# Performance work log

Measured on AMD Instinct MI355X. Metric: run time of the kernel, lower is better.

Reference implementation:

```python
import jax, jax.numpy as jnp
import numpy as np

NEAR, FAR, N_SAMPLES = 1.0, 6.0, 64
FAR_APPEND = 1000.0


def setup_inputs() -> dict:
    key = jax.random.key(0)
    ks = jax.random.split(key, 8)
    B, R = 2, 4096
    # pixel coords in a 128x128 image
    x_pix = jax.random.uniform(ks[0], (B, R, 2), dtype=jnp.float32) * 128.0
    # plausible pinhole intrinsics (fx=fy=128, cx=cy=64)
    K = jnp.array([[128.0, 0.0, 64.0], [0.0, 128.0, 64.0], [0.0, 0.0, 1.0]], dtype=jnp.float32)
    intrinsics = jnp.tile(K[None], (B, 1, 1))
    # identity rotation, small translation cam2world
    c2w = jnp.eye(4, dtype=jnp.float32).at[:3, 3].set(jnp.array([0.1, -0.2, 0.5]))
    cam2world = jnp.tile(c2w[None], (B, 1, 1))
    H = 256
    W1 = jax.random.normal(ks[1], (3, H), dtype=jnp.float32) / np.sqrt(3.0)
    b1 = jnp.zeros((H,), jnp.float32)
    W2 = jax.random.normal(ks[2], (H, H), dtype=jnp.float32) / np.sqrt(H)
    b2 = jnp.zeros((H,), jnp.float32)
    W3 = jax.random.normal(ks[3], (H, 4), dtype=jnp.float32) / np.sqrt(H)
    b3 = jnp.zeros((4,), jnp.float32)
    return {"x_pix": x_pix, "intrinsics": intrinsics, "cam2world": cam2world,
            "W1": W1, "b1": b1, "W2": W2, "b2": b2, "W3": W3, "b3": b3}


def _radiance_field(pts, W1, b1, W2, b2, W3, b3):
    # pts: (B, N, 3) -> sigma (B, N, 1), rad (B, N, 3)
    h = jax.nn.relu(pts @ W1 + b1)
    h = jax.nn.relu(h @ W2 + b2)
    o = h @ W3 + b3
    return jax.nn.relu(o[..., :1]), jax.nn.sigmoid(o[..., 1:])


def _get_world_rays(x_pix, intrinsics, cam2world):
    B, R, _ = x_pix.shape
    inv_K = jnp.linalg.inv(intrinsics)  # (B,3,3)
    xy_hom = jnp.concatenate([x_pix, jnp.ones((B, R, 1), x_pix.dtype)], axis=-1)  # (B,R,3)
    dirs_cam = jnp.einsum("bij,brj->bri", inv_K, xy_hom)  # unnormalized cam-frame dirs
    dirs_hom = jnp.concatenate([dirs_cam, jnp.zeros((B, R, 1), x_pix.dtype)], axis=-1)  # w=0 vector
    dirs_world = jnp.einsum("bij,brj->bri", cam2world, dirs_hom)[..., :3]
    origins = jnp.broadcast_to(cam2world[:, None, :3, 3], (B, R, 3))
    return origins, dirs_world


def _volume_integral(z_vals, sigmas, radiances):
    # z_vals: (S,); sigmas: (B,R,S,1); radiances: (B,R,S,3)
    dists = jnp.diff(z_vals, append=jnp.array([FAR_APPEND], z_vals.dtype))  # (S,)
    alpha = 1.0 - jnp.exp(-sigmas * dists[None, None, :, None])  # (B,R,S,1)
    Ts = jnp.cumprod(1.0 - alpha, axis=2)  # inclusive cumprod, matching torch
    weights = alpha * Ts  # (B,R,S,1)
    rgb = jnp.sum(weights * radiances, axis=2)  # (B,R,3)
    depth_map = jnp.einsum("brsv,s->brv", weights, z_vals)  # (B,R,1)
    return rgb, depth_map, weights


def reference(x_pix, intrinsics, cam2world, W1, b1, W2, b2, W3, b3):
    B, R = x_pix.shape[0], x_pix.shape[1]
    ros, rds = _get_world_rays(x_pix, intrinsics, cam2world)
    z_vals = jnp.linspace(NEAR, FAR, N_SAMPLES, dtype=x_pix.dtype)  # (S,)
    pts = ros[:, :, None, :] + rds[:, :, None, :] * z_vals[None, None, :, None]  # (B,R,S,3)
    pts = pts.reshape(B, -1, 3)
    sigma, rad = _radiance_field(pts, W1, b1, W2, b2, W3, b3)
    sigma = sigma.reshape(B, R, N_SAMPLES, 1)
    rad = rad.reshape(B, R, N_SAMPLES, 3)
    rgb, depth_map, weights = _volume_integral(z_vals, sigma, rad)
    accum = jnp.sum(weights, axis=-2)  # (B,R,1)
    rgb = rgb + (1.0 - accum)  # white background
    return rgb, depth_map
```

## Files before the change

kernel.cpp:

```cpp
#include <hip/hip_runtime.h>

typedef unsigned short u16;
typedef _Float16 f16x8 __attribute__((ext_vector_type(8)));
typedef float    f32x4  __attribute__((ext_vector_type(4)));
typedef float    f32x16 __attribute__((ext_vector_type(16)));

#define NRAYS 8192

#define WS_W2T  0
#define WS_B2   131072
#define WS_W3   132096
#define WS_B3   136192
#define WS_W1   136208
#define WS_B1   139280
#define WS_INTR 140304
#define WS_C2W  140384

__device__ __forceinline__ float bf2f(u16 u){
  union { unsigned int i; float f; } v; v.i = ((unsigned int)u) << 16; return v.f;
}
__device__ __forceinline__ u16 f2h(float f){
  union { _Float16 h; u16 u; } v; v.h = (_Float16)f;
  return v.u;
}
__device__ __forceinline__ int detect_bf16(const void* intr){
  return (((const u16*)intr)[0] == 0x4300u) ? 1 : 0;
}

__device__ __forceinline__ void conv_arr(const void* src, float* dst, int n, int bf, int tid){
  if (bf){
    const u16* s = (const u16*)src;
    for (int i = tid; i < n; i += 256) dst[i] = bf2f(s[i]);
  } else {
    const float* s = (const float*)src;
    for (int i = tid; i < n; i += 256) dst[i] = s[i];
  }
}

__global__ void prep(const void* __restrict__ W2, const void* __restrict__ W1,
                     const void* __restrict__ b1, const void* __restrict__ b2,
                     const void* __restrict__ W3, const void* __restrict__ b3,
                     const void* __restrict__ intr, const void* __restrict__ c2w,
                     char* __restrict__ ws)
{
  const int bf = detect_bf16(intr);
  const int t = threadIdx.x;
  if (blockIdx.x == 16){
    conv_arr(W1,  (float*)(ws + WS_W1),  768,  bf, t);
    conv_arr(b1,  (float*)(ws + WS_B1),  256,  bf, t);
    conv_arr(b2,  (float*)(ws + WS_B2),  256,  bf, t);
    conv_arr(W3,  (float*)(ws + WS_W3),  1024, bf, t);
    conv_arr(b3,  (float*)(ws + WS_B3),  4,    bf, t);
    conv_arr(intr,(float*)(ws + WS_INTR),18,   bf, t);
    conv_arr(c2w, (float*)(ws + WS_C2W), 32,   bf, t);
    return;
  }
  __shared__ u16 tile[64][72];
  const int bx = blockIdx.x & 3;
  const int by = blockIdx.x >> 2;
  const int c = t & 63, rb = t >> 6;
  u16* W2T = (u16*)(ws + WS_W2T);
  #pragma unroll
  for (int rr = 0; rr < 64; rr += 4){
    int k = bx*64 + rr + rb;
    int n = by*64 + c;
    float v = bf ? bf2f(((const u16*)W2)[k*256 + n]) : ((const float*)W2)[k*256 + n];
    tile[rr + rb][c] = f2h(v);
  }
  __syncthreads();
  #pragma unroll
  for (int rr = 0; rr < 64; rr += 4){
    int n = by*64 + rr + rb;
    int k = bx*64 + c;
    W2T[n*256 + k] = tile[c][rr + rb];
  }
}

__global__ __launch_bounds__(256, 2) void nerf_fused(
    const void* __restrict__ x_pix,
    const void* __restrict__ intr,
    const char* __restrict__ ws,
    float* __restrict__ out)
{
  __shared__ __align__(16) u16   h1s[128 * 256];
  __shared__ __align__(16) float obuf[4 * 128 * 4];

  const int tid = threadIdx.x;
  const int l   = tid & 63;
  const int w   = tid >> 6;
  const int ray = w >> 1;
  const int rayg = blockIdx.x * 2 + ray;
  const int bb   = rayg >> 12;
  const int bf   = detect_bf16(intr);

  const float* intrf = (const float*)(ws + WS_INTR);
  const float* c2wf  = (const float*)(ws + WS_C2W);
  const float* W1f   = (const float*)(ws + WS_W1);
  const float* b1f   = (const float*)(ws + WS_B1);
  const float* b2f   = (const float*)(ws + WS_B2);
  const float* W3f   = (const float*)(ws + WS_W3);
  const u16*   W2T   = (const u16*)(ws + WS_W2T);

  float px, py;
  if (bf){
    px = bf2f(((const u16*)x_pix)[rayg*2 + 0]);
    py = bf2f(((const u16*)x_pix)[rayg*2 + 1]);
  } else {
    px = ((const float*)x_pix)[rayg*2 + 0];
    py = ((const float*)x_pix)[rayg*2 + 1];
  }
  float Ka[9], Mm[16];
  #pragma unroll
  for (int i = 0; i < 9;  i++) Ka[i] = intrf[bb*9  + i];
  #pragma unroll
  for (int i = 0; i < 16; i++) Mm[i] = c2wf[bb*16 + i];
  float a = Ka[0], b_ = Ka[1], c = Ka[2];
  float d = Ka[3], e  = Ka[4], f = Ka[5];
  float g = Ka[6], h_ = Ka[7], i9 = Ka[8];
  float det = a*(e*i9 - f*h_) - b_*(d*i9 - f*g) + c*(d*h_ - e*g);
  float inv = 1.0f / det;
  float i00 = (e*i9 - f*h_)*inv, i01 = (c*h_ - b_*i9)*inv, i02 = (b_*f - c*e)*inv;
  float i10 = (f*g - d*i9)*inv, i11 = (a*i9 - c*g)*inv, i12 = (c*d - a*f)*inv;
  float i20 = (d*h_ - e*g)*inv, i21 = (b_*g - a*h_)*inv, i22 = (a*e - b_*d)*inv;
  float dcx = i00*px + i01*py + i02;
  float dcy = i10*px + i11*py + i12;
  float dcz = i20*px + i21*py + i22;
  float dx = Mm[0]*dcx + Mm[1]*dcy + Mm[2]*dcz;
  float dy = Mm[4]*dcx + Mm[5]*dcy + Mm[6]*dcz;
  float dz = Mm[8]*dcx + Mm[9]*dcy + Mm[10]*dcz;
  float ox = Mm[3], oy = Mm[7], oz = Mm[11];

  const int kbase = (w & 1)*128 + l*2;
  float aa0, aa1, gg0, gg1;
  {
    float2 r0 = *(const float2*)(W1f + kbase);
    float2 r1 = *(const float2*)(W1f + 256 + kbase);
    float2 r2 = *(const float2*)(W1f + 512 + kbase);
    float2 rb = *(const float2*)(b1f + kbase);
    aa0 = ox*r0.x + oy*r1.x + oz*r2.x + rb.x;
    aa1 = ox*r0.y + oy*r1.y + oz*r2.y + rb.y;
    gg0 = dx*r0.x + dy*r1.x + dz*r2.x;
    gg1 = dx*r0.y + dy*r1.y + dz*r2.y;
  }
  const float step = 5.0f / 63.0f;
  const int chunk_w = ((w & 1) << 4) + (l >> 2);
  const int sub_b   = (l & 3) << 2;
  {
    char* hb = (char*)h1s + (ray*64)*512;
    #pragma unroll 8
    for (int s = 0; s < 64; s++){
      float z = 1.0f + step * (float)s;
      u16 e0 = f2h(fmaxf(fmaf(gg0, z, aa0), 0.0f));
      u16 e1 = f2h(fmaxf(fmaf(gg1, z, aa1), 0.0f));
      unsigned pk = (unsigned)e0 | ((unsigned)e1 << 16);
      *(unsigned*)(hb + s*512 + ((chunk_w ^ (s & 7)) << 4) + sub_b) = pk;
    }
  }
  __syncthreads();

  const int l31 = l & 31;
  const int h   = l >> 5;
  const int m7  = l31 & 7;
  const int nbase = w * 64;

  f32x16 acc[2][4];
  #pragma unroll
  for (int nt = 0; nt < 2; nt++)
    #pragma unroll
    for (int mt = 0; mt < 4; mt++)
      acc[nt][mt] = (f32x16){0.f,0.f,0.f,0.f,0.f,0.f,0.f,0.f,
                             0.f,0.f,0.f,0.f,0.f,0.f,0.f,0.f};

  const u16* Arow = W2T + (nbase + l31)*256 + h*8;
  const char* hbase = (const char*)h1s;

  f16x8 a_cur[2];
  a_cur[0] = *(const f16x8*)(Arow);
  a_cur[1] = *(const f16x8*)(Arow + 32*256);

  #pragma unroll
  for (int t = 0; t < 16; t++){
    f16x8 a_nxt[2];
    if (t < 15){
      a_nxt[0] = *(const f16x8*)(Arow + (t+1)*16);
      a_nxt[1] = *(const f16x8*)(Arow + 32*256 + (t+1)*16);
    }
    const int swz = ((2*t + h) ^ m7) << 4;
    f16x8 bfr[4];
    #pragma unroll
    for (int mt = 0; mt < 4; mt++)
      bfr[mt] = *(const f16x8*)(hbase + (mt*32 + l31)*512 + swz);
    #pragma unroll
    for (int nt = 0; nt < 2; nt++)
      #pragma unroll
      for (int mt = 0; mt < 4; mt++)
        acc[nt][mt] = __builtin_amdgcn_mfma_f32_32x32x16_f16(
            a_cur[nt], bfr[mt], acc[nt][mt], 0, 0, 0);
    if (t < 15){ a_cur[0] = a_nxt[0]; a_cur[1] = a_nxt[1]; }
  }

  f32x4 o_m[4];
  #pragma unroll
  for (int mt = 0; mt < 4; mt++) o_m[mt] = (f32x4){0.f,0.f,0.f,0.f};

  #pragma unroll
  for (int nt = 0; nt < 2; nt++){
    #pragma unroll
    for (int gq = 0; gq < 4; gq++){
      const int n0 = nbase + nt*32 + gq*8 + h*4;
      f32x4 b2v = *(const f32x4*)(b2f + n0);
      f32x4 w30 = *(const f32x4*)(W3f + n0*4);
      f32x4 w31 = *(const f32x4*)(W3f + (n0+1)*4);
      f32x4 w32 = *(const f32x4*)(W3f + (n0+2)*4);
      f32x4 w33 = *(const f32x4*)(W3f + (n0+3)*4);
      #pragma unroll
      for (int mt = 0; mt < 4; mt++){
        float h0 = fmaxf(acc[nt][mt][gq*4+0] + b2v.x, 0.0f);
        float h1 = fmaxf(acc[nt][mt][gq*4+1] + b2v.y, 0.0f);
        float h2 = fmaxf(acc[nt][mt][gq*4+2] + b2v.z, 0.0f);
        float h3 = fmaxf(acc[nt][mt][gq*4+3] + b2v.w, 0.0f);
        o_m[mt] = o_m[mt] + h0*w30 + h1*w31 + h2*w32 + h3*w33;
      }
    }
  }

  #pragma unroll
  for (int mt = 0; mt < 4; mt++)
    #pragma unroll
    for (int j = 0; j < 4; j++){
      float v = o_m[mt][j];
      v += __shfl_xor(v, 32, 64);
      o_m[mt][j] = v;
    }

  if (h == 0){
    #pragma unroll
    for (int mt = 0; mt < 4; mt++)
      *(f32x4*)&obuf[(w*128 + mt*32 + l31)*4] = o_m[mt];
  }
  __syncthreads();

  if (w < 2){
    const int m = w*64 + l;
    const f32x4* ob4 = (const f32x4*)obuf;
    f32x4 oj  = ob4[m] + ob4[128 + m] + ob4[256 + m] + ob4[384 + m];
    f32x4 b3v = *(const f32x4*)(ws + WS_B3);
    float o_s0 = oj.x + b3v.x;
    float o_s1 = oj.y + b3v.y;
    float o_s2 = oj.z + b3v.z;
    float o_s3 = oj.w + b3v.w;

    const float zc    = 1.0f + step * (float)l;
    const float znext = (l == 63) ? 1000.0f : (1.0f + step * (float)(l + 1));
    const float dist  = znext - zc;
    float sigma = fmaxf(o_s0, 0.0f);
    float alpha = 1.0f - __expf(-sigma * dist);
    float t = 1.0f - alpha;
    #pragma unroll
    for (int sh = 1; sh < 64; sh <<= 1){
      float u = __shfl_up(t, sh, 64);
      if (l >= sh) t *= u;
    }
    float wgt = alpha * t;
    float r0 = 1.0f / (1.0f + __expf(-o_s1));
    float r1 = 1.0f / (1.0f + __expf(-o_s2));
    float r2 = 1.0f / (1.0f + __expf(-o_s3));
    float s0 = wgt*r0, s1 = wgt*r1, s2 = wgt*r2, sw = wgt, sz = wgt*zc;
    #pragma unroll
    for (int sh = 1; sh < 64; sh <<= 1){
      s0 += __shfl_xor(s0, sh, 64);
      s1 += __shfl_xor(s1, sh, 64);
      s2 += __shfl_xor(s2, sh, 64);
      sw += __shfl_xor(sw, sh, 64);
      sz += __shfl_xor(sz, sh, 64);
    }
    if (l == 0){
      const int rg = blockIdx.x*2 + w;
      float bg = 1.0f - sw;
      out[rg*3 + 0] = s0 + bg;
      out[rg*3 + 1] = s1 + bg;
      out[rg*3 + 2] = s2 + bg;
      out[3*NRAYS + rg] = sz;
    }
  }
}

extern "C" void kernel_launch(void* const* d_in, const int* in_sizes, int n_in,
                              void* d_out, int out_size, void* d_ws, size_t ws_size,
                              hipStream_t stream)
{
  const void* x_pix = d_in[0];
  const void* intr  = d_in[1];
  const void* c2w   = d_in[2];
  const void* W1    = d_in[3];
  const void* b1    = d_in[4];
  const void* W2    = d_in[5];
  const void* b2    = d_in[6];
  const void* W3    = d_in[7];
  const void* b3    = d_in[8];
  float* outp = (float*)d_out;
  char*  ws   = (char*)d_ws;

  hipLaunchKernelGGL(prep, dim3(17), dim3(256), 0, stream,
                     W2, W1, b1, b2, W3, b3, intr, c2w, ws);
  hipLaunchKernelGGL(nerf_fused, dim3(NRAYS/2), dim3(256), 0, stream,
                     x_pix, intr, ws, outp);
}
```

Before: 177.0 us.

## Make fused NeRF kernel persistent with W2 fragments held in registers

The launch shrinks from 4096 blocks to 512. Each block now loops over 8 ray pairs and loads its whole slice of the transposed W2 into registers once, instead of streaming it from global memory for every ray pair. The W1 and b1 slices are also hoisted out of the loop. The aim is to cut repeated weight traffic and per-block setup, at the cost of much higher register pressure (128 VGPRs of weights plus the accumulators) and less block-level parallelism to hide latency.

```diff
diff --git a/kernel.cpp b/kernel.cpp
--- a/kernel.cpp
+++ b/kernel.cpp
@@ -88,10 +88,7 @@
   const int tid = threadIdx.x;
   const int l   = tid & 63;
   const int w   = tid >> 6;
-  const int ray = w >> 1;
-  const int rayg = blockIdx.x * 2 + ray;
-  const int bb   = rayg >> 12;
-  const int bf   = detect_bf16(intr);
+  const int bf  = detect_bf16(intr);
 
   const float* intrf = (const float*)(ws + WS_INTR);
   const float* c2wf  = (const float*)(ws + WS_C2W);
@@ -101,186 +98,189 @@
   const float* W3f   = (const float*)(ws + WS_W3);
   const u16*   W2T   = (const u16*)(ws + WS_W2T);
 
-  float px, py;
-  if (bf){
-    px = bf2f(((const u16*)x_pix)[rayg*2 + 0]);
-    py = bf2f(((const u16*)x_pix)[rayg*2 + 1]);
-  } else {
-    px = ((const float*)x_pix)[rayg*2 + 0];
-    py = ((const float*)x_pix)[rayg*2 + 1];
-  }
-  float Ka[9], Mm[16];
-  #pragma unroll
-  for (int i = 0; i < 9;  i++) Ka[i] = intrf[bb*9  + i];
-  #pragma unroll
-  for (int i = 0; i < 16; i++) Mm[i] = c2wf[bb*16 + i];
-  float a = Ka[0], b_ = Ka[1], c = Ka[2];
-  float d = Ka[3], e  = Ka[4], f = Ka[5];
-  float g = Ka[6], h_ = Ka[7], i9 = Ka[8];
-  float det = a*(e*i9 - f*h_) - b_*(d*i9 - f*g) + c*(d*h_ - e*g);
-  float inv = 1.0f / det;
-  float i00 = (e*i9 - f*h_)*inv, i01 = (c*h_ - b_*i9)*inv, i02 = (b_*f - c*e)*inv;
-  float i10 = (f*g - d*i9)*inv, i11 = (a*i9 - c*g)*inv, i12 = (c*d - a*f)*inv;
-  float i20 = (d*h_ - e*g)*inv, i21 = (b_*g - a*h_)*inv, i22 = (a*e - b_*d)*inv;
-  float dcx = i00*px + i01*py + i02;
-  float dcy = i10*px + i11*py + i12;
-  float dcz = i20*px + i21*py + i22;
-  float dx = Mm[0]*dcx + Mm[1]*dcy + Mm[2]*dcz;
-  float dy = Mm[4]*dcx + Mm[5]*dcy + Mm[6]*dcz;
-  float dz = Mm[8]*dcx + Mm[9]*dcy + Mm[10]*dcz;
-  float ox = Mm[3], oy = Mm[7], oz = Mm[11];
-
-  const int kbase = (w & 1)*128 + l*2;
-  float aa0, aa1, gg0, gg1;
-  {
-    float2 r0 = *(const float2*)(W1f + kbase);
-    float2 r1 = *(const float2*)(W1f + 256 + kbase);
-    float2 r2 = *(const float2*)(W1f + 512 + kbase);
-    float2 rb = *(const float2*)(b1f + kbase);
-    aa0 = ox*r0.x + oy*r1.x + oz*r2.x + rb.x;
-    aa1 = ox*r0.y + oy*r1.y + oz*r2.y + rb.y;
-    gg0 = dx*r0.x + dy*r1.x + dz*r2.x;
-    gg1 = dx*r0.y + dy*r1.y + dz*r2.y;
-  }
-  const float step = 5.0f / 63.0f;
-  const int chunk_w = ((w & 1) << 4) + (l >> 2);
-  const int sub_b   = (l & 3) << 2;
-  {
-    char* hb = (char*)h1s + (ray*64)*512;
-    #pragma unroll 8
-    for (int s = 0; s < 64; s++){
-      float z = 1.0f + step * (float)s;
-      u16 e0 = f2h(fmaxf(fmaf(gg0, z, aa0), 0.0f));
-      u16 e1 = f2h(fmaxf(fmaf(gg1, z, aa1), 0.0f));
-      unsigned pk = (unsigned)e0 | ((unsigned)e1 << 16);
-      *(unsigned*)(hb + s*512 + ((chunk_w ^ (s & 7)) << 4) + sub_b) = pk;
-    }
-  }
-  __syncthreads();
-
   const int l31 = l & 31;
   const int h   = l >> 5;
   const int m7  = l31 & 7;
   const int nbase = w * 64;
 
-  f32x16 acc[2][4];
-  #pragma unroll
-  for (int nt = 0; nt < 2; nt++)
+  f16x8 aw[2][16];
+  {
+    const u16* Arow = W2T + (nbase + l31)*256 + h*8;
+    #pragma unroll
+    for (int nt = 0; nt < 2; nt++)
+      #pragma unroll
+      for (int kt = 0; kt < 16; kt++)
+        aw[nt][kt] = *(const f16x8*)(Arow + nt*32*256 + kt*16);
+  }
+
+  const int kbase = (w & 1)*128 + l*2;
+  const float2 r0 = *(const float2*)(W1f + kbase);
+  const float2 r1 = *(const float2*)(W1f + 256 + kbase);
+  const float2 r2 = *(const float2*)(W1f + 512 + kbase);
+  const float2 rbv = *(const float2*)(b1f + kbase);
+  const int chunk_w = ((w & 1) << 4) + (l >> 2);
+  const int sub_b   = (l & 3) << 2;
+  const float step = 5.0f / 63.0f;
+
+  #pragma unroll 1
+  for (int it = 0; it < 8; it++){
+    const int pr   = it*512 + blockIdx.x;
+    const int rayg = pr*2 + (w >> 1);
+    const int bb   = rayg >> 12;
+
+    float px, py;
+    if (bf){
+      px = bf2f(((const u16*)x_pix)[rayg*2 + 0]);
+      py = bf2f(((const u16*)x_pix)[rayg*2 + 1]);
+    } else {
+      px = ((const float*)x_pix)[rayg*2 + 0];
+      py = ((const float*)x_pix)[rayg*2 + 1];
+    }
+    float Ka[9], Mm[16];
+    #pragma unroll
+    for (int i = 0; i < 9;  i++) Ka[i] = intrf[bb*9  + i];
+    #pragma unroll
+    for (int i = 0; i < 16; i++) Mm[i] = c2wf[bb*16 + i];
+    float a = Ka[0], b_ = Ka[1], c = Ka[2];
+    float d = Ka[3], e  = Ka[4], f = Ka[5];
+    float g = Ka[6], h_ = Ka[7], i9 = Ka[8];
+    float det = a*(e*i9 - f*h_) - b_*(d*i9 - f*g) + c*(d*h_ - e*g);
+    float inv = 1.0f / det;
+    float i00 = (e*i9 - f*h_)*inv, i01 = (c*h_ - b_*i9)*inv, i02 = (b_*f - c*e)*inv;
+    float i10 = (f*g - d*i9)*inv, i11 = (a*i9 - c*g)*inv, i12 = (c*d - a*f)*inv;
+    float i20 = (d*h_ - e*g)*inv, i21 = (b_*g - a*h_)*inv, i22 = (a*e - b_*d)*inv;
+    float dcx = i00*px + i01*py + i02;
+    float dcy = i10*px + i11*py + i12;
+    float dcz = i20*px + i21*py + i22;
+    float dx = Mm[0]*dcx + Mm[1]*dcy + Mm[2]*dcz;
+    float dy = Mm[4]*dcx + Mm[5]*dcy + Mm[6]*dcz;
+    float dz = Mm[8]*dcx + Mm[9]*dcy + Mm[10]*dcz;
+    float ox = Mm[3], oy = Mm[7], oz = Mm[11];
+
+    float aa0 = ox*r0.x + oy*r1.x + oz*r2.x + rbv.x;
+    float aa1 = ox*r0.y + oy*r1.y + oz*r2.y + rbv.y;
+    float gg0 = dx*r0.x + dy*r1.x + dz*r2.x;
+    float gg1 = dx*r0.y + dy*r1.y + dz*r2.y;
+    {
+      char* hb = (char*)h1s + ((w >> 1)*64)*512;
+      #pragma unroll 8
+      for (int s = 0; s < 64; s++){
+        float z = 1.0f + step * (float)s;
+        u16 e0 = f2h(fmaxf(fmaf(gg0, z, aa0), 0.0f));
+        u16 e1 = f2h(fmaxf(fmaf(gg1, z, aa1), 0.0f));
+        unsigned pk = (unsigned)e0 | ((unsigned)e1 << 16);
+        *(unsigned*)(hb + s*512 + ((chunk_w ^ (s & 7)) << 4) + sub_b) = pk;
+      }
+    }
+    __syncthreads();
+
+    f32x16 acc[2][4];
+    #pragma unroll
+    for (int nt = 0; nt < 2; nt++)
+      #pragma unroll
+      for (int mt = 0; mt < 4; mt++)
+        acc[nt][mt] = (f32x16){0.f,0.f,0.f,0.f,0.f,0.f,0.f,0.f,
+                               0.f,0.f,0.f,0.f,0.f,0.f,0.f,0.f};
+
+    const char* hbase = (const char*)h1s;
+    #pragma unroll
+    for (int kt = 0; kt < 16; kt++){
+      const int swz = ((2*kt + h) ^ m7) << 4;
+      f16x8 bfr[4];
+      #pragma unroll
+      for (int mt = 0; mt < 4; mt++)
+        bfr[mt] = *(const f16x8*)(hbase + (mt*32 + l31)*512 + swz);
+      #pragma unroll
+      for (int nt = 0; nt < 2; nt++)
+        #pragma unroll
+        for (int mt = 0; mt < 4; mt++)
+          acc[nt][mt] = __builtin_amdgcn_mfma_f32_32x32x16_f16(
+              aw[nt][kt], bfr[mt], acc[nt][mt], 0, 0, 0);
+    }
+
+    f32x4 o_m[4];
+    #pragma unroll
+    for (int mt = 0; mt < 4; mt++) o_m[mt] = (f32x4){0.f,0.f,0.f,0.f};
+
+    #pragma unroll
+    for (int nt = 0; nt < 2; nt++){
+      #pragma unroll
+      for (int gq = 0; gq < 4; gq++){
+        const int n0 = nbase + nt*32 + gq*8 + h*4;
+        f32x4 b2v = *(const f32x4*)(b2f + n0);
+        f32x4 w30 = *(const f32x4*)(W3f + n0*4);
+        f32x4 w31 = *(const f32x4*)(W3f + (n0+1)*4);
+        f32x4 w32 = *(const f32x4*)(W3f + (n0+2)*4);
+        f32x4 w33 = *(const f32x4*)(W3f + (n0+3)*4);
+        #pragma unroll
+        for (int mt = 0; mt < 4; mt++){
+          float h0 = fmaxf(acc[nt][mt][gq*4+0] + b2v.x, 0.0f);
+          float h1 = fmaxf(acc[nt][mt][gq*4+1] + b2v.y, 0.0f);
+          float h2 = fmaxf(acc[nt][mt][gq*4+2] + b2v.z, 0.0f);
+          float h3 = fmaxf(acc[nt][mt][gq*4+3] + b2v.w, 0.0f);
+          o_m[mt] = o_m[mt] + h0*w30 + h1*w31 + h2*w32 + h3*w33;
+        }
+      }
+    }
+
     #pragma unroll
     for (int mt = 0; mt < 4; mt++)
-      acc[nt][mt] = (f32x16){0.f,0.f,0.f,0.f,0.f,0.f,0.f,0.f,
-                             0.f,0.f,0.f,0.f,0.f,0.f,0.f,0.f};
-
-  const u16* Arow = W2T + (nbase + l31)*256 + h*8;
-  const char* hbase = (const char*)h1s;
-
-  f16x8 a_cur[2];
-  a_cur[0] = *(const f16x8*)(Arow);
-  a_cur[1] = *(const f16x8*)(Arow + 32*256);
-
-  #pragma unroll
-  for (int t = 0; t < 16; t++){
-    f16x8 a_nxt[2];
-    if (t < 15){
-      a_nxt[0] = *(const f16x8*)(Arow + (t+1)*16);
-      a_nxt[1] = *(const f16x8*)(Arow + 32*256 + (t+1)*16);
-    }
-    const int swz = ((2*t + h) ^ m7) << 4;
-    f16x8 bfr[4];
-    #pragma unroll
-    for (int mt = 0; mt < 4; mt++)
-      bfr[mt] = *(const f16x8*)(hbase + (mt*32 + l31)*512 + swz);
-    #pragma unroll
-    for (int nt = 0; nt < 2; nt++)
+      #pragma unroll
+      for (int j = 0; j < 4; j++){
+        float v = o_m[mt][j];
+        v += __shfl_xor(v, 32, 64);
+        o_m[mt][j] = v;
+      }
+
+    if (h == 0){
       #pragma unroll
       for (int mt = 0; mt < 4; mt++)
-        acc[nt][mt] = __builtin_amdgcn_mfma_f32_32x32x16_f16(
-            a_cur[nt], bfr[mt], acc[nt][mt], 0, 0, 0);
-    if (t < 15){ a_cur[0] = a_nxt[0]; a_cur[1] = a_nxt[1]; }
-  }
-
-  f32x4 o_m[4];
-  #pragma unroll
-  for (int mt = 0; mt < 4; mt++) o_m[mt] = (f32x4){0.f,0.f,0.f,0.f};
-
-  #pragma unroll
-  for (int nt = 0; nt < 2; nt++){
-    #pragma unroll
-    for (int gq = 0; gq < 4; gq++){
-      const int n0 = nbase + nt*32 + gq*8 + h*4;
-      f32x4 b2v = *(const f32x4*)(b2f + n0);
-      f32x4 w30 = *(const f32x4*)(W3f + n0*4);
-      f32x4 w31 = *(const f32x4*)(W3f + (n0+1)*4);
-      f32x4 w32 = *(const f32x4*)(W3f + (n0+2)*4);
-      f32x4 w33 = *(const f32x4*)(W3f + (n0+3)*4);
-      #pragma unroll
-      for (int mt = 0; mt < 4; mt++){
-        float h0 = fmaxf(acc[nt][mt][gq*4+0] + b2v.x, 0.0f);
-        float h1 = fmaxf(acc[nt][mt][gq*4+1] + b2v.y, 0.0f);
-        float h2 = fmaxf(acc[nt][mt][gq*4+2] + b2v.z, 0.0f);
-        float h3 = fmaxf(acc[nt][mt][gq*4+3] + b2v.w, 0.0f);
-        o_m[mt] = o_m[mt] + h0*w30 + h1*w31 + h2*w32 + h3*w33;
-      }
-    }
-  }
-
-  #pragma unroll
-  for (int mt = 0; mt < 4; mt++)
-    #pragma unroll
-    for (int j = 0; j < 4; j++){
-      float v = o_m[mt][j];
-      v += __shfl_xor(v, 32, 64);
-      o_m[mt][j] = v;
-    }
-
-  if (h == 0){
-    #pragma unroll
-    for (int mt = 0; mt < 4; mt++)
-      *(f32x4*)&obuf[(w*128 + mt*32 + l31)*4] = o_m[mt];
-  }
-  __syncthreads();
-
-  if (w < 2){
-    const int m = w*64 + l;
-    const f32x4* ob4 = (const f32x4*)obuf;
-    f32x4 oj  = ob4[m] + ob4[128 + m] + ob4[256 + m] + ob4[384 + m];
-    f32x4 b3v = *(const f32x4*)(ws + WS_B3);
-    float o_s0 = oj.x + b3v.x;
-    float o_s1 = oj.y + b3v.y;
-    float o_s2 = oj.z + b3v.z;
-    float o_s3 = oj.w + b3v.w;
-
-    const float zc    = 1.0f + step * (float)l;
-    const float znext = (l == 63) ? 1000.0f : (1.0f + step * (float)(l + 1));
-    const float dist  = znext - zc;
-    float sigma = fmaxf(o_s0, 0.0f);
-    float alpha = 1.0f - __expf(-sigma * dist);
-    float t = 1.0f - alpha;
-    #pragma unroll
-    for (int sh = 1; sh < 64; sh <<= 1){
-      float u = __shfl_up(t, sh, 64);
-      if (l >= sh) t *= u;
-    }
-    float wgt = alpha * t;
-    float r0 = 1.0f / (1.0f + __expf(-o_s1));
-    float r1 = 1.0f / (1.0f + __expf(-o_s2));
-    float r2 = 1.0f / (1.0f + __expf(-o_s3));
-    float s0 = wgt*r0, s1 = wgt*r1, s2 = wgt*r2, sw = wgt, sz = wgt*zc;
-    #pragma unroll
-    for (int sh = 1; sh < 64; sh <<= 1){
-      s0 += __shfl_xor(s0, sh, 64);
-      s1 += __shfl_xor(s1, sh, 64);
-      s2 += __shfl_xor(s2, sh, 64);
-      sw += __shfl_xor(sw, sh, 64);
-      sz += __shfl_xor(sz, sh, 64);
-    }
-    if (l == 0){
-      const int rg = blockIdx.x*2 + w;
-      float bg = 1.0f - sw;
-      out[rg*3 + 0] = s0 + bg;
-      out[rg*3 + 1] = s1 + bg;
-      out[rg*3 + 2] = s2 + bg;
-      out[3*NRAYS + rg] = sz;
+        *(f32x4*)&obuf[(w*128 + mt*32 + l31)*4] = o_m[mt];
+    }
+    __syncthreads();
+
+    if (w < 2){
+      const int m = w*64 + l;
+      const f32x4* ob4 = (const f32x4*)obuf;
+      f32x4 oj  = ob4[m] + ob4[128 + m] + ob4[256 + m] + ob4[384 + m];
+      f32x4 b3v = *(const f32x4*)(ws + WS_B3);
+      float o_s0 = oj.x + b3v.x;
+      float o_s1 = oj.y + b3v.y;
+      float o_s2 = oj.z + b3v.z;
+      float o_s3 = oj.w + b3v.w;
+
+      const float zc    = 1.0f + step * (float)l;
+      const float znext = (l == 63) ? 1000.0f : (1.0f + step * (float)(l + 1));
+      const float dist  = znext - zc;
+      float sigma = fmaxf(o_s0, 0.0f);
+      float alpha = 1.0f - __expf(-sigma * dist);
+      float tr = 1.0f - alpha;
+      #pragma unroll
+      for (int sh = 1; sh < 64; sh <<= 1){
+        float u = __shfl_up(tr, sh, 64);
+        if (l >= sh) tr *= u;
+      }
+      float wgt = alpha * tr;
+      float q0 = 1.0f / (1.0f + __expf(-o_s1));
+      float q1 = 1.0f / (1.0f + __expf(-o_s2));
+      float q2 = 1.0f / (1.0f + __expf(-o_s3));
+      float s0 = wgt*q0, s1 = wgt*q1, s2 = wgt*q2, sw = wgt, sz = wgt*zc;
+      #pragma unroll
+      for (int sh = 1; sh < 64; sh <<= 1){
+        s0 += __shfl_xor(s0, sh, 64);
+        s1 += __shfl_xor(s1, sh, 64);
+        s2 += __shfl_xor(s2, sh, 64);
+        sw += __shfl_xor(sw, sh, 64);
+        sz += __shfl_xor(sz, sh, 64);
+      }
+      if (l == 0){
+        const int rg = pr*2 + w;
+        float bg = 1.0f - sw;
+        out[rg*3 + 0] = s0 + bg;
+        out[rg*3 + 1] = s1 + bg;
+        out[rg*3 + 2] = s2 + bg;
+        out[3*NRAYS + rg] = sz;
+      }
     }
   }
 }
@@ -303,6 +303,6 @@
 
   hipLaunchKernelGGL(prep, dim3(17), dim3(256), 0, stream,
                      W2, W1, b1, b2, W3, b3, intr, c2w, ws);
-  hipLaunchKernelGGL(nerf_fused, dim3(NRAYS/2), dim3(256), 0, stream,
+  hipLaunchKernelGGL(nerf_fused, dim3(512), dim3(256), 0, stream,
                      x_pix, intr, ws, outp);
 }
```

New measurement: 289.1 us. +63.4%, slower.
